# Optimization experiments

Hardware: AMD Instinct MI355X
Metric: run time of the kernel (lower is better)

## Reference

```python
import jax, jax.numpy as jnp
import numpy as np

N_NODES = 100000
NEG_SLOPE = 0.01


def setup_inputs() -> dict:
    key = jax.random.key(0)
    k1, k2, k3, k4 = jax.random.split(key, 4)
    E = 1600000
    x = jax.random.normal(k1, (N_NODES, 256), dtype=jnp.float32)
    edge_index = jax.random.randint(k2, (2, E), 0, N_NODES, dtype=jnp.int64)
    # Glorot-ish init for GCN linear weights
    W1 = jax.random.normal(k3, (256, 128), dtype=jnp.float32) / np.sqrt(256.0)
    b1 = jnp.zeros((128,), dtype=jnp.float32)
    W2 = jax.random.normal(k4, (128, 64), dtype=jnp.float32) / np.sqrt(128.0)
    b2 = jnp.zeros((64,), dtype=jnp.float32)
    return {"x": x, "edge_index": edge_index, "W1": W1, "b1": b1, "W2": W2, "b2": b2}


def _gcn_norm(edge_index, n_nodes):
    # Add self-loops (PyG GCNConv default), symmetric normalization.
    loops = jnp.arange(n_nodes, dtype=edge_index.dtype)
    src = jnp.concatenate([edge_index[0], loops])
    dst = jnp.concatenate([edge_index[1], loops])
    deg = jax.ops.segment_sum(jnp.ones_like(dst, dtype=jnp.float32), dst,
                              num_segments=n_nodes)
    dinv = jnp.where(deg > 0, 1.0 / jnp.sqrt(deg), 0.0)
    norm = dinv[src] * dinv[dst]  # [E + N]
    return src, dst, norm


def _gcn_conv(h, W, b, src, dst, norm, n_nodes):
    h = h @ W                              # [N, out] linear transform first
    msg = h[src] * norm[:, None]           # gather + edge weighting
    agg = jax.ops.segment_sum(msg, dst, num_segments=n_nodes)  # scatter-add
    return agg + b


def reference(x, edge_index, W1, b1, W2, b2):
    n = x.shape[0]
    src, dst, norm = _gcn_norm(edge_index, n)
    h = _gcn_conv(x, W1, b1, src, dst, norm, n)
    h = jnp.where(h >= 0, h, NEG_SLOPE * h)  # leaky_relu, slope 0.01
    return _gcn_conv(h, W2, b2, src, dst, norm, n)
```

## Files before the change

kernel.cpp:

```cpp
#include <hip/hip_runtime.h>
#include <hip/hip_bf16.h>
#include <stdint.h>

#define GPART 512
#define BSHIFT 9
#define BSIZE 512
#define MAXNB 512

typedef short short8 __attribute__((ext_vector_type(8)));
typedef float f32x4 __attribute__((ext_vector_type(4)));
union U4S8 { uint4 u; short8 s; };

static __device__ __forceinline__ float bflo(uint32_t h){ return __uint_as_float(h << 16); }
static __device__ __forceinline__ float bfhi(uint32_t h){ return __uint_as_float(h & 0xFFFF0000u); }
static __device__ __forceinline__ uint32_t f2bf_bits(float f){
  uint32_t u = __float_as_uint(f);
  return (u + 0x7FFFu + ((u >> 16) & 1u)) >> 16;
}
static __device__ __forceinline__ uint32_t pack2bf(float lo, float hi){
  return f2bf_bits(lo) | (f2bf_bits(hi) << 16);
}

static __device__ __forceinline__ void gemm1_tile(const float* __restrict__ X,
    const uint4* __restrict__ W1f, unsigned short* __restrict__ H1, int n,
    int row0, char* smem, int tid){
  float (*xs)[256] = (float (*)[256])smem;
  int wid = tid >> 6, lane = tid & 63;
  #pragma unroll
  for (int i = 0; i < 8; ++i){
    int r = wid*8 + i;
    int gr = min(row0 + r, n - 1);
    const float* gsrc = X + (size_t)gr*256 + 4*(lane ^ (r & 7));
    __builtin_amdgcn_global_load_lds(
        (const __attribute__((address_space(1))) unsigned int*)gsrc,
        (__attribute__((address_space(3))) unsigned int*)(&xs[r][0]),
        16, 0, 0);
  }
  __syncthreads();
  int mhalf = wid & 1, nh = wid >> 1;
  int rA = lane & 15, kg = lane >> 4;
  int lrow = mhalf*16 + rA;
  f32x4 acc[4];
  #pragma unroll
  for (int nt = 0; nt < 4; ++nt) acc[nt] = (f32x4){0.f, 0.f, 0.f, 0.f};
  #pragma unroll
  for (int ks = 0; ks < 8; ++ks){
    int g0 = ks*8 + kg*2;
    float4 f0 = *(const float4*)&xs[lrow][4*( g0      ^ (rA & 7))];
    float4 f1 = *(const float4*)&xs[lrow][4*((g0 + 1) ^ (rA & 7))];
    U4S8 a;
    a.u.x = pack2bf(f0.x, f0.y); a.u.y = pack2bf(f0.z, f0.w);
    a.u.z = pack2bf(f1.x, f1.y); a.u.w = pack2bf(f1.z, f1.w);
    #pragma unroll
    for (int nt = 0; nt < 4; ++nt){
      U4S8 b; b.u = W1f[(ks*8 + nh*4 + nt)*64 + lane];
      acc[nt] = __builtin_amdgcn_mfma_f32_16x16x32_bf16(a.s, b.s, acc[nt], 0, 0, 0);
    }
  }
  int rowbase = row0 + mhalf*16 + kg*4;
  #pragma unroll
  for (int r = 0; r < 4; ++r){
    int row = rowbase + r;
    if (row < n){
      #pragma unroll
      for (int nt = 0; nt < 4; ++nt)
        H1[(size_t)row*128 + (nh*4 + nt)*16 + rA] = (unsigned short)f2bf_bits(acc[nt][r]);
    }
  }
}

__global__ __launch_bounds__(256) void k_fat_hist(const int* __restrict__ dst, int E, int NB,
    int* __restrict__ gHist,
    const float* __restrict__ X, const uint4* __restrict__ W1f,
    unsigned short* __restrict__ H1, int n, int g1base, int nbuild){
  __shared__ __align__(16) char smem[32768];
  int tid = threadIdx.x;
  if ((int)blockIdx.x >= nbuild){
    int row0 = (g1base + (int)blockIdx.x - nbuild) * 32;
    gemm1_tile(X, W1f, H1, n, row0, smem, tid);
    return;
  }
  int* lh = (int*)smem;
  int blk = blockIdx.x;
  for (int i = tid; i < NB; i += 256) lh[i] = 0;
  __syncthreads();
  int chunk = (E + GPART - 1) / GPART;
  int e0 = blk * chunk, e1 = min(E, e0 + chunk);
  for (int e = e0 + tid; e < e1; e += 256)
    atomicAdd(&lh[dst[e] >> BSHIFT], 1);
  __syncthreads();
  for (int i = tid; i < NB; i += 256) gHist[i * GPART + blk] = lh[i];
}

__global__ __launch_bounds__(64) void k_scanA(int* __restrict__ gHist,
    int* __restrict__ bucketTotal){
  int b = blockIdx.x;
  int lane = threadIdx.x;
  int carry = 0;
  #pragma unroll
  for (int r = 0; r < GPART/64; ++r){
    int v = gHist[b*GPART + r*64 + lane];
    int pref = v;
    #pragma unroll
    for (int off = 1; off < 64; off <<= 1){ int t = __shfl_up(pref, off); if (lane >= off) pref += t; }
    int tot = __shfl(pref, 63);
    gHist[b*GPART + r*64 + lane] = carry + pref - v;
    carry += tot;
  }
  if (lane == 0) bucketTotal[b] = carry;
}

__global__ __launch_bounds__(64) void k_scanB(const int* __restrict__ bucketTotal, int NB,
    int* __restrict__ bucketBase){
  int lane = threadIdx.x;
  int carry = 0;
  for (int r = 0; r*64 < NB; ++r){
    int idx = r*64 + lane;
    int v = (idx < NB) ? bucketTotal[idx] : 0;
    int pref = v;
    #pragma unroll
    for (int off = 1; off < 64; off <<= 1){ int t = __shfl_up(pref, off); if (lane >= off) pref += t; }
    int tot = __shfl(pref, 63);
    if (idx < NB) bucketBase[idx] = carry + pref - v;
    carry += tot;
  }
}

__global__ __launch_bounds__(256) void k_fat_scatter(const int* __restrict__ src,
    const int* __restrict__ dst, int E, int NB,
    const int* __restrict__ gHist, const int* __restrict__ bucketBase,
    uint32_t* __restrict__ edgesP,
    const float* __restrict__ X, const uint4* __restrict__ W1f,
    unsigned short* __restrict__ H1, int n, int g1base, int nbuild){
  __shared__ __align__(16) char smem[32768];
  int tid = threadIdx.x;
  if ((int)blockIdx.x >= nbuild){
    int row0 = (g1base + (int)blockIdx.x - nbuild) * 32;
    gemm1_tile(X, W1f, H1, n, row0, smem, tid);
    return;
  }
  int* lpos = (int*)smem;
  int blk = blockIdx.x;
  for (int i = tid; i < NB; i += 256) lpos[i] = 0;
  __syncthreads();
  int chunk = (E + GPART - 1) / GPART;
  int e0 = blk * chunk, e1 = min(E, e0 + chunk);
  for (int e = e0 + tid; e < e1; e += 256){
    int s = src[e], d = dst[e];
    int b = d >> BSHIFT;
    int o = atomicAdd(&lpos[b], 1);
    int pos = bucketBase[b] + gHist[b*GPART + blk] + o;
    edgesP[pos] = (uint32_t)s | ((uint32_t)(d & (BSIZE-1)) << 23);
  }
}

__global__ __launch_bounds__(256) void k_fat_p1(const uint32_t* __restrict__ edgesP,
    const int* __restrict__ bucketBase, const int* __restrict__ bucketTotal,
    int n, int* __restrict__ start, int* __restrict__ cnt, float* __restrict__ dinv,
    const float* __restrict__ X, const uint4* __restrict__ W1f,
    unsigned short* __restrict__ H1, int g1base, int nbuild){
  __shared__ __align__(16) char smem[32768];
  int tid = threadIdx.x;
  if ((int)blockIdx.x >= nbuild){
    int row0 = (g1base + (int)blockIdx.x - nbuild) * 32;
    gemm1_tile(X, W1f, H1, n, row0, smem, tid);
    return;
  }
  int* cnt_l   = (int*)smem;
  int* start_l = (int*)(smem + BSIZE*4);
  int b = blockIdx.x;
  int base = bucketBase[b], total = bucketTotal[b];
  int d0 = b << BSHIFT;
  for (int i = tid; i < BSIZE; i += 256) cnt_l[i] = 0;
  __syncthreads();
  for (int i = tid; i < total; i += 256)
    atomicAdd(&cnt_l[edgesP[base + i] >> 23], 1);
  __syncthreads();
  if (tid < 64){
    int lane = tid, carry = 0;
    #pragma unroll
    for (int r = 0; r < BSIZE/64; ++r){
      int v = cnt_l[r*64 + lane];
      int pref = v;
      #pragma unroll
      for (int off = 1; off < 64; off <<= 1){ int t = __shfl_up(pref, off); if (lane >= off) pref += t; }
      int tot = __shfl(pref, 63);
      start_l[r*64 + lane] = carry + pref - v;
      carry += tot;
    }
  }
  __syncthreads();
  for (int i = tid; i < BSIZE; i += 256){
    int d = d0 + i;
    if (d < n){
      int c = cnt_l[i];
      cnt[d] = c;
      start[d] = base + start_l[i];
      dinv[d] = rsqrtf((float)(c + 1));
    }
  }
}

__global__ __launch_bounds__(256) void k_fat_p2(const uint32_t* __restrict__ edgesP,
    const int* __restrict__ bucketBase, const int* __restrict__ bucketTotal,
    const int* __restrict__ start, const float* __restrict__ dinv,
    int2* __restrict__ csr,
    const float* __restrict__ X, const uint4* __restrict__ W1f,
    unsigned short* __restrict__ H1, int n, int g1base, int nbuild){
  __shared__ __align__(16) char smem[32768];
  int tid = threadIdx.x;
  if ((int)blockIdx.x >= nbuild){
    int row0 = (g1base + (int)blockIdx.x - nbuild) * 32;
    gemm1_tile(X, W1f, H1, n, row0, smem, tid);
    return;
  }
  int* fp = (int*)smem;
  int b = blockIdx.x;
  int base = bucketBase[b], total = bucketTotal[b];
  int d0 = b << BSHIFT;
  for (int i = tid; i < BSIZE; i += 256) fp[i] = 0;
  __syncthreads();
  for (int i = tid; i < total; i += 256){
    uint32_t w = edgesP[base + i];
    int dl = (int)(w >> 23);
    int s = (int)(w & 0x7FFFFFu);
    int p = atomicAdd(&fp[dl], 1);
    float wt = dinv[s] * dinv[d0 + dl];
    csr[start[d0 + dl] + p] = make_int2(s, __float_as_int(wt));
  }
}

__global__ __launch_bounds__(256) void k_packW(const float* __restrict__ W,
    uint4* __restrict__ Wf, int K, int Nc){
  int s = blockIdx.x * 256 + threadIdx.x;
  int total = (K >> 5) * (Nc >> 4) * 64;
  if (s >= total) return;
  int lane = s & 63;
  int frag = s >> 6;
  int NT = Nc >> 4;
  int nt = frag % NT, ks = frag / NT;
  int col = nt*16 + (lane & 15);
  int k0  = ks*32 + (lane >> 4)*8;
  float v[8];
  #pragma unroll
  for (int e = 0; e < 8; ++e) v[e] = W[(size_t)(k0 + e)*Nc + col];
  uint4 u;
  u.x = pack2bf(v[0], v[1]); u.y = pack2bf(v[2], v[3]);
  u.z = pack2bf(v[4], v[5]); u.w = pack2bf(v[6], v[7]);
  Wf[s] = u;
}

__global__ __launch_bounds__(256) void k_agg1(const uint4* __restrict__ H1,
    const int2* __restrict__ csr,
    const int* __restrict__ start, const int* __restrict__ cnt,
    const float* __restrict__ dinv, const float* __restrict__ b1,
    uint4* __restrict__ A1, int n){
  int w = (int)((blockIdx.x * blockDim.x + threadIdx.x) >> 6);
  int lane = threadIdx.x & 63;
  if (w >= n) return;
  int g = lane >> 4, li = lane & 15;
  float dw = dinv[w];
  float sw = (g == 0) ? dw * dw : 0.f;
  uint4 hs = H1[(size_t)w*16 + li];
  float acc[8];
  acc[0]=sw*bflo(hs.x); acc[1]=sw*bfhi(hs.x); acc[2]=sw*bflo(hs.y); acc[3]=sw*bfhi(hs.y);
  acc[4]=sw*bflo(hs.z); acc[5]=sw*bfhi(hs.z); acc[6]=sw*bflo(hs.w); acc[7]=sw*bfhi(hs.w);
  int e0 = start[w], deg = cnt[w];
  for (int base = 0; base < deg; base += 64){
    int nin = min(64, deg - base);
    int2 ew = (lane < nin) ? csr[e0 + base + lane] : make_int2(0, 0);
    for (int j = 0; j < nin; j += 8){
      int   sA = __shfl(ew.x, j + g);
      float wA = __uint_as_float((uint32_t)__shfl(ew.y, j + g));
      int   sB = __shfl(ew.x, j + 4 + g);
      float wB = __uint_as_float((uint32_t)__shfl(ew.y, j + 4 + g));
      uint4 hA = H1[(size_t)sA*16 + li];
      uint4 hB = H1[(size_t)sB*16 + li];
      acc[0]=fmaf(wA,bflo(hA.x),acc[0]); acc[1]=fmaf(wA,bfhi(hA.x),acc[1]);
      acc[2]=fmaf(wA,bflo(hA.y),acc[2]); acc[3]=fmaf(wA,bfhi(hA.y),acc[3]);
      acc[4]=fmaf(wA,bflo(hA.z),acc[4]); acc[5]=fmaf(wA,bfhi(hA.z),acc[5]);
      acc[6]=fmaf(wA,bflo(hA.w),acc[6]); acc[7]=fmaf(wA,bfhi(hA.w),acc[7]);
      acc[0]=fmaf(wB,bflo(hB.x),acc[0]); acc[1]=fmaf(wB,bfhi(hB.x),acc[1]);
      acc[2]=fmaf(wB,bflo(hB.y),acc[2]); acc[3]=fmaf(wB,bfhi(hB.y),acc[3]);
      acc[4]=fmaf(wB,bflo(hB.z),acc[4]); acc[5]=fmaf(wB,bfhi(hB.z),acc[5]);
      acc[6]=fmaf(wB,bflo(hB.w),acc[6]); acc[7]=fmaf(wB,bfhi(hB.w),acc[7]);
    }
  }
  #pragma unroll
  for (int e = 0; e < 8; ++e){
    acc[e] += __shfl_xor(acc[e], 16);
    acc[e] += __shfl_xor(acc[e], 32);
  }
  float4 bA = *(const float4*)&b1[li*8];
  float4 bB = *(const float4*)&b1[li*8 + 4];
  acc[0]+=bA.x; acc[1]+=bA.y; acc[2]+=bA.z; acc[3]+=bA.w;
  acc[4]+=bB.x; acc[5]+=bB.y; acc[6]+=bB.z; acc[7]+=bB.w;
  #pragma unroll
  for (int e = 0; e < 8; ++e) acc[e] = (acc[e] >= 0.f) ? acc[e] : 0.01f * acc[e];
  if (g == 0){
    uint4 o;
    o.x = pack2bf(acc[0], acc[1]); o.y = pack2bf(acc[2], acc[3]);
    o.z = pack2bf(acc[4], acc[5]); o.w = pack2bf(acc[6], acc[7]);
    A1[(size_t)w*16 + li] = o;
  }
}

__global__ __launch_bounds__(256) void k_gemm2_mfma(const uint4* __restrict__ A1,
    const uint4* __restrict__ W2f, unsigned short* __restrict__ H2, int n){
  int wv = (int)((blockIdx.x * 256u + threadIdx.x) >> 6);
  int lane = threadIdx.x & 63;
  int row0 = wv * 16;
  if (row0 >= n) return;
  int rA = lane & 15, kg = lane >> 4;
  f32x4 acc[4];
  #pragma unroll
  for (int nt = 0; nt < 4; ++nt) acc[nt] = (f32x4){0.f, 0.f, 0.f, 0.f};
  int r0 = min(row0 + rA, n - 1);
  const uint4* arow = A1 + (size_t)r0*16 + kg;
  uint4 u = arow[0];
  #pragma unroll
  for (int ks = 0; ks < 4; ++ks){
    U4S8 a; a.u = u;
    if (ks < 3) u = arow[(ks+1)*4];
    #pragma unroll
    for (int nt = 0; nt < 4; ++nt){
      U4S8 b; b.u = W2f[(ks*4 + nt)*64 + lane];
      acc[nt] = __builtin_amdgcn_mfma_f32_16x16x32_bf16(a.s, b.s, acc[nt], 0, 0, 0);
    }
  }
  #pragma unroll
  for (int r = 0; r < 4; ++r){
    int row = row0 + kg*4 + r;
    if (row < n){
      #pragma unroll
      for (int nt = 0; nt < 4; ++nt)
        H2[(size_t)row*64 + nt*16 + rA] = (unsigned short)f2bf_bits(acc[nt][r]);
    }
  }
}

__global__ __launch_bounds__(256) void k_agg2(const uint4* __restrict__ H2,
    const int2* __restrict__ csr,
    const int* __restrict__ start, const int* __restrict__ cnt,
    const float* __restrict__ dinv, const float* __restrict__ b2,
    float* __restrict__ out, int n){
  int w = (int)((blockIdx.x * blockDim.x + threadIdx.x) >> 6);
  int lane = threadIdx.x & 63;
  if (w >= n) return;
  int g = lane >> 3, li = lane & 7;
  float dw = dinv[w];
  float sw = (g == 0) ? dw * dw : 0.f;
  uint4 hs = H2[(size_t)w*8 + li];
  float acc[8];
  acc[0]=sw*bflo(hs.x); acc[1]=sw*bfhi(hs.x); acc[2]=sw*bflo(hs.y); acc[3]=sw*bfhi(hs.y);
  acc[4]=sw*bflo(hs.z); acc[5]=sw*bfhi(hs.z); acc[6]=sw*bflo(hs.w); acc[7]=sw*bfhi(hs.w);
  int e0 = start[w], deg = cnt[w];
  for (int base = 0; base < deg; base += 64){
    int nin = min(64, deg - base);
    int2 ew = (lane < nin) ? csr[e0 + base + lane] : make_int2(0, 0);
    for (int j = 0; j < nin; j += 16){
      int   sA = __shfl(ew.x, j + g);
      float wA = __uint_as_float((uint32_t)__shfl(ew.y, j + g));
      int   sB = __shfl(ew.x, j + 8 + g);
      float wB = __uint_as_float((uint32_t)__shfl(ew.y, j + 8 + g));
      uint4 hA = H2[(size_t)sA*8 + li];
      uint4 hB = H2[(size_t)sB*8 + li];
      acc[0]=fmaf(wA,bflo(hA.x),acc[0]); acc[1]=fmaf(wA,bfhi(hA.x),acc[1]);
      acc[2]=fmaf(wA,bflo(hA.y),acc[2]); acc[3]=fmaf(wA,bfhi(hA.y),acc[3]);
      acc[4]=fmaf(wA,bflo(hA.z),acc[4]); acc[5]=fmaf(wA,bfhi(hA.z),acc[5]);
      acc[6]=fmaf(wA,bflo(hA.w),acc[6]); acc[7]=fmaf(wA,bfhi(hA.w),acc[7]);
      acc[0]=fmaf(wB,bflo(hB.x),acc[0]); acc[1]=fmaf(wB,bfhi(hB.x),acc[1]);
      acc[2]=fmaf(wB,bflo(hB.y),acc[2]); acc[3]=fmaf(wB,bfhi(hB.y),acc[3]);
      acc[4]=fmaf(wB,bflo(hB.z),acc[4]); acc[5]=fmaf(wB,bfhi(hB.z),acc[5]);
      acc[6]=fmaf(wB,bflo(hB.w),acc[6]); acc[7]=fmaf(wB,bfhi(hB.w),acc[7]);
    }
  }
  #pragma unroll
  for (int e = 0; e < 8; ++e){
    acc[e] += __shfl_xor(acc[e], 8);
    acc[e] += __shfl_xor(acc[e], 16);
    acc[e] += __shfl_xor(acc[e], 32);
  }
  float4 bA = *(const float4*)&b2[li*8];
  float4 bB = *(const float4*)&b2[li*8 + 4];
  acc[0]+=bA.x; acc[1]+=bA.y; acc[2]+=bA.z; acc[3]+=bA.w;
  acc[4]+=bB.x; acc[5]+=bB.y; acc[6]+=bB.z; acc[7]+=bB.w;
  if (g == 0){
    float4 o0 = make_float4(acc[0], acc[1], acc[2], acc[3]);
    float4 o1 = make_float4(acc[4], acc[5], acc[6], acc[7]);
    *(float4*)&out[(size_t)w*64 + li*8]     = o0;
    *(float4*)&out[(size_t)w*64 + li*8 + 4] = o1;
  }
}

extern "C" void kernel_launch(void* const* d_in, const int* in_sizes, int n_in,
                              void* d_out, int out_size, void* d_ws, size_t ws_size,
                              hipStream_t stream){
  const float* x  = (const float*)d_in[0];
  const int*   ei = (const int*)d_in[1];
  const float* W1 = (const float*)d_in[2];
  const float* b1 = (const float*)d_in[3];
  const float* W2 = (const float*)d_in[4];
  const float* b2 = (const float*)d_in[5];
  float* out = (float*)d_out;

  int N = in_sizes[0] / 256;
  int E = in_sizes[1] / 2;
  int NB = (N + BSIZE - 1) >> BSHIFT;

  char* p = (char*)d_ws;
  uint32_t* H1   = (uint32_t*)p;  p += (size_t)N*64*4;
  uint32_t* A1   = (uint32_t*)p;  p += (size_t)N*64*4;
  uint32_t* H2   = (uint32_t*)p;  p += (size_t)N*32*4;
  uint32_t* edgesP=(uint32_t*)p;  p += (size_t)E*4;
  int2* csr      = (int2*)p;      p += (size_t)E*8;
  int* gHist     = (int*)p;       p += (size_t)NB*GPART*4;
  int* bucketTotal=(int*)p;       p += (size_t)((NB+63)&~63)*4;
  int* bucketBase= (int*)p;       p += (size_t)((NB+63)&~63)*4;
  uint4* W1f     = (uint4*)p;     p += 8*8*64*16;
  uint4* W2f     = (uint4*)p;     p += 4*4*64*16;
  int* start     = (int*)p;       p += (size_t)N*4;
  int* cnt       = (int*)p;       p += (size_t)N*4;
  float* dinv    = (float*)p;     p += (size_t)N*4;

  const int* srcIdx = ei;
  const int* dstIdx = ei + E;

  unsigned short* H1u = (unsigned short*)H1;

  int G1 = (N + 31) / 32;
  int sA = (int)((long)G1 * 20 / 100);
  int sB = (int)((long)G1 * 33 / 100);
  int sC = (int)((long)G1 * 18 / 100);
  int sD = G1 - sA - sB - sC;

  int nW2 = (N + 15) / 16;
  int nG2Blocks = (nW2 + 3) / 4;
  int nNodeBlocks = (N + 3) / 4;

  k_packW<<<(8*8*64 + 255)/256, 256, 0, stream>>>(W1, W1f, 256, 128);
  k_packW<<<(4*4*64 + 255)/256, 256, 0, stream>>>(W2, W2f, 128, 64);
  k_fat_hist<<<GPART + sA, 256, 0, stream>>>(dstIdx, E, NB, gHist,
      x, W1f, H1u, N, 0, GPART);
  k_scanA<<<NB, 64, 0, stream>>>(gHist, bucketTotal);
  k_scanB<<<1, 64, 0, stream>>>(bucketTotal, NB, bucketBase);
  k_fat_scatter<<<GPART + sB, 256, 0, stream>>>(srcIdx, dstIdx, E, NB, gHist, bucketBase,
      edgesP, x, W1f, H1u, N, sA, GPART);
  k_fat_p1<<<NB + sC, 256, 0, stream>>>(edgesP, bucketBase, bucketTotal, N, start, cnt, dinv,
      x, W1f, H1u, sA + sB, NB);
  k_fat_p2<<<NB + sD, 256, 0, stream>>>(edgesP, bucketBase, bucketTotal, start, dinv, csr,
      x, W1f, H1u, N, sA + sB + sC, NB);
  k_agg1<<<nNodeBlocks, 256, 0, stream>>>((const uint4*)H1, csr, start, cnt, dinv, b1, (uint4*)A1, N);
  k_gemm2_mfma<<<nG2Blocks, 256, 0, stream>>>((const uint4*)A1, W2f, (unsigned short*)H2, N);
  k_agg2<<<nNodeBlocks, 256, 0, stream>>>((const uint4*)H2, csr, start, cnt, dinv, b2, out, N);
}
```

Before: 212.4 us.

## Fuse CSR build passes and store source-only CSR, computing edge weights in aggregation

Merges the two per-bucket CSR-building kernels into one, so the counting/scan and the fill happen in a single launch using shared-memory start offsets. The CSR now stores only the source index (4 bytes instead of 8). Edge weights are recomputed in both aggregation kernels from dinv[src]*dinv[dst]. This removes one launch and one re-read of edgesP, and halves CSR traffic. In exchange it adds a dependent dinv gather per edge during aggregation, and the GEMM1 tile split is rebalanced over three launches.

```diff
diff --git a/kernel.cpp b/kernel.cpp
--- a/kernel.cpp
+++ b/kernel.cpp
@@ -154,9 +154,10 @@
   }
 }
 
-__global__ __launch_bounds__(256) void k_fat_p1(const uint32_t* __restrict__ edgesP,
+__global__ __launch_bounds__(256) void k_fat_p12(const uint32_t* __restrict__ edgesP,
     const int* __restrict__ bucketBase, const int* __restrict__ bucketTotal,
     int n, int* __restrict__ start, int* __restrict__ cnt, float* __restrict__ dinv,
+    int* __restrict__ csr,
     const float* __restrict__ X, const uint4* __restrict__ W1f,
     unsigned short* __restrict__ H1, int g1base, int nbuild){
   __shared__ __align__(16) char smem[32768];
@@ -167,11 +168,12 @@
     return;
   }
   int* cnt_l   = (int*)smem;
-  int* start_l = (int*)(smem + BSIZE*4);
+  int* start_l = (int*)(smem + 2048);
+  int* fp      = (int*)(smem + 4096);
   int b = blockIdx.x;
   int base = bucketBase[b], total = bucketTotal[b];
   int d0 = b << BSHIFT;
-  for (int i = tid; i < BSIZE; i += 256) cnt_l[i] = 0;
+  for (int i = tid; i < BSIZE; i += 256){ cnt_l[i] = 0; fp[i] = 0; }
   __syncthreads();
   for (int i = tid; i < total; i += 256)
     atomicAdd(&cnt_l[edgesP[base + i] >> 23], 1);
@@ -199,34 +201,12 @@
       dinv[d] = rsqrtf((float)(c + 1));
     }
   }
-}
-
-__global__ __launch_bounds__(256) void k_fat_p2(const uint32_t* __restrict__ edgesP,
-    const int* __restrict__ bucketBase, const int* __restrict__ bucketTotal,
-    const int* __restrict__ start, const float* __restrict__ dinv,
-    int2* __restrict__ csr,
-    const float* __restrict__ X, const uint4* __restrict__ W1f,
-    unsigned short* __restrict__ H1, int n, int g1base, int nbuild){
-  __shared__ __align__(16) char smem[32768];
-  int tid = threadIdx.x;
-  if ((int)blockIdx.x >= nbuild){
-    int row0 = (g1base + (int)blockIdx.x - nbuild) * 32;
-    gemm1_tile(X, W1f, H1, n, row0, smem, tid);
-    return;
-  }
-  int* fp = (int*)smem;
-  int b = blockIdx.x;
-  int base = bucketBase[b], total = bucketTotal[b];
-  int d0 = b << BSHIFT;
-  for (int i = tid; i < BSIZE; i += 256) fp[i] = 0;
-  __syncthreads();
   for (int i = tid; i < total; i += 256){
     uint32_t w = edgesP[base + i];
     int dl = (int)(w >> 23);
     int s = (int)(w & 0x7FFFFFu);
     int p = atomicAdd(&fp[dl], 1);
-    float wt = dinv[s] * dinv[d0 + dl];
-    csr[start[d0 + dl] + p] = make_int2(s, __float_as_int(wt));
+    csr[base + start_l[dl] + p] = s;
   }
 }
 
@@ -251,7 +231,7 @@
 }
 
 __global__ __launch_bounds__(256) void k_agg1(const uint4* __restrict__ H1,
-    const int2* __restrict__ csr,
+    const int* __restrict__ csr,
     const int* __restrict__ start, const int* __restrict__ cnt,
     const float* __restrict__ dinv, const float* __restrict__ b1,
     uint4* __restrict__ A1, int n){
@@ -268,12 +248,13 @@
   int e0 = start[w], deg = cnt[w];
   for (int base = 0; base < deg; base += 64){
     int nin = min(64, deg - base);
-    int2 ew = (lane < nin) ? csr[e0 + base + lane] : make_int2(0, 0);
+    int sE = (lane < nin) ? csr[e0 + base + lane] : 0;
+    float dvE = (lane < nin) ? dinv[sE] : 0.f;
     for (int j = 0; j < nin; j += 8){
-      int   sA = __shfl(ew.x, j + g);
-      float wA = __uint_as_float((uint32_t)__shfl(ew.y, j + g));
-      int   sB = __shfl(ew.x, j + 4 + g);
-      float wB = __uint_as_float((uint32_t)__shfl(ew.y, j + 4 + g));
+      int   sA = __shfl(sE, j + g);
+      float wA = __shfl(dvE, j + g) * dw;
+      int   sB = __shfl(sE, j + 4 + g);
+      float wB = __shfl(dvE, j + 4 + g) * dw;
       uint4 hA = H1[(size_t)sA*16 + li];
       uint4 hB = H1[(size_t)sB*16 + li];
       acc[0]=fmaf(wA,bflo(hA.x),acc[0]); acc[1]=fmaf(wA,bfhi(hA.x),acc[1]);
@@ -340,7 +321,7 @@
 }
 
 __global__ __launch_bounds__(256) void k_agg2(const uint4* __restrict__ H2,
-    const int2* __restrict__ csr,
+    const int* __restrict__ csr,
     const int* __restrict__ start, const int* __restrict__ cnt,
     const float* __restrict__ dinv, const float* __restrict__ b2,
     float* __restrict__ out, int n){
@@ -357,12 +338,13 @@
   int e0 = start[w], deg = cnt[w];
   for (int base = 0; base < deg; base += 64){
     int nin = min(64, deg - base);
-    int2 ew = (lane < nin) ? csr[e0 + base + lane] : make_int2(0, 0);
+    int sE = (lane < nin) ? csr[e0 + base + lane] : 0;
+    float dvE = (lane < nin) ? dinv[sE] : 0.f;
     for (int j = 0; j < nin; j += 16){
-      int   sA = __shfl(ew.x, j + g);
-      float wA = __uint_as_float((uint32_t)__shfl(ew.y, j + g));
-      int   sB = __shfl(ew.x, j + 8 + g);
-      float wB = __uint_as_float((uint32_t)__shfl(ew.y, j + 8 + g));
+      int   sA = __shfl(sE, j + g);
+      float wA = __shfl(dvE, j + g) * dw;
+      int   sB = __shfl(sE, j + 8 + g);
+      float wB = __shfl(dvE, j + 8 + g) * dw;
       uint4 hA = H2[(size_t)sA*8 + li];
       uint4 hB = H2[(size_t)sB*8 + li];
       acc[0]=fmaf(wA,bflo(hA.x),acc[0]); acc[1]=fmaf(wA,bfhi(hA.x),acc[1]);
@@ -413,7 +395,7 @@
   uint32_t* A1   = (uint32_t*)p;  p += (size_t)N*64*4;
   uint32_t* H2   = (uint32_t*)p;  p += (size_t)N*32*4;
   uint32_t* edgesP=(uint32_t*)p;  p += (size_t)E*4;
-  int2* csr      = (int2*)p;      p += (size_t)E*8;
+  int* csr       = (int*)p;       p += (size_t)E*4;
   int* gHist     = (int*)p;       p += (size_t)NB*GPART*4;
   int* bucketTotal=(int*)p;       p += (size_t)((NB+63)&~63)*4;
   int* bucketBase= (int*)p;       p += (size_t)((NB+63)&~63)*4;
@@ -430,9 +412,8 @@
 
   int G1 = (N + 31) / 32;
   int sA = (int)((long)G1 * 20 / 100);
-  int sB = (int)((long)G1 * 33 / 100);
-  int sC = (int)((long)G1 * 18 / 100);
-  int sD = G1 - sA - sB - sC;
+  int sB = (int)((long)G1 * 40 / 100);
+  int sC = G1 - sA - sB;
 
   int nW2 = (N + 15) / 16;
   int nG2Blocks = (nW2 + 3) / 4;
@@ -446,10 +427,8 @@
   k_scanB<<<1, 64, 0, stream>>>(bucketTotal, NB, bucketBase);
   k_fat_scatter<<<GPART + sB, 256, 0, stream>>>(srcIdx, dstIdx, E, NB, gHist, bucketBase,
       edgesP, x, W1f, H1u, N, sA, GPART);
-  k_fat_p1<<<NB + sC, 256, 0, stream>>>(edgesP, bucketBase, bucketTotal, N, start, cnt, dinv,
-      x, W1f, H1u, sA + sB, NB);
-  k_fat_p2<<<NB + sD, 256, 0, stream>>>(edgesP, bucketBase, bucketTotal, start, dinv, csr,
-      x, W1f, H1u, N, sA + sB + sC, NB);
+  k_fat_p12<<<NB + sC, 256, 0, stream>>>(edgesP, bucketBase, bucketTotal, N, start, cnt, dinv,
+      csr, x, W1f, H1u, sA + sB, NB);
   k_agg1<<<nNodeBlocks, 256, 0, stream>>>((const uint4*)H1, csr, start, cnt, dinv, b1, (uint4*)A1, N);
   k_gemm2_mfma<<<nG2Blocks, 256, 0, stream>>>((const uint4*)A1, W2f, (unsigned short*)H2, N);
   k_agg2<<<nNodeBlocks, 256, 0, stream>>>((const uint4*)H2, csr, start, cnt, dinv, b2, out, N);
```

Result: faster. 201.7 us, median of 2 (-5.0%).
